# Performance work log

Measured on AMD Instinct MI355X. Metric: run time of the kernel, lower is better.

The kernel has to match this reference:

```python
import jax, jax.numpy as jnp
import numpy as np

B, C, A = 4, 8, 9            # batch, num_classes, anchors per location
IMG = 512.0                   # image spatial size (square)
FEATS = [64, 32, 16, 8, 4]    # FPN feature map sizes
STRIDES = [8, 16, 32, 64, 128]
TOPK = 1000                   # topk_candidates_per_level
SCORE_THRESH = 0.05
NMS_THRESH = 0.5
DETS = 300                    # detections_per_img
BBOX_CLIP = float(np.log(1000.0 / 16.0))  # standard BoxCoder dw/dh clamp


def _make_anchors(f, stride):
    # 3 aspect ratios x 3 octave scales = 9 anchors per location (torchvision-style)
    base = stride * 4.0
    ratios = np.array([0.5, 1.0, 2.0])
    scales = np.array([2.0 ** 0, 2.0 ** (1.0 / 3.0), 2.0 ** (2.0 / 3.0)])
    ws, hs = [], []
    for r in ratios:
        for sc in scales:
            area = (base * sc) ** 2
            w = np.sqrt(area / r)
            ws.append(w)
            hs.append(w * r)
    ws = np.array(ws)
    hs = np.array(hs)
    shifts = (np.arange(f) + 0.5) * stride
    cx, cy = np.meshgrid(shifts, shifts, indexing='ij')  # H-major, matches map flatten
    cx = cx.reshape(-1)[:, None]
    cy = cy.reshape(-1)[:, None]
    boxes = np.stack([cx - ws / 2, cy - hs / 2, cx + ws / 2, cy + hs / 2], axis=-1)
    return boxes.reshape(-1, 4).astype(np.float32)  # [f*f*A, 4], location-major


def setup_inputs() -> dict:
    key = jax.random.key(0)
    inp = {}
    for i, (f, s) in enumerate(zip(FEATS, STRIDES)):
        k1 = jax.random.fold_in(key, 2 * i)
        k2 = jax.random.fold_in(key, 2 * i + 1)
        inp[f'cls_{i}'] = jax.random.normal(k1, (B, C * A, f, f), jnp.float32)
        inp[f'reg_{i}'] = 0.2 * jax.random.normal(k2, (B, 4 * A, f, f), jnp.float32)
        inp[f'anchors_{i}'] = jnp.asarray(_make_anchors(f, s))
    return inp


def _decode(reg, anc):
    # BoxCoder.decode with weights (1,1,1,1)
    aw = anc[..., 2] - anc[..., 0]
    ah = anc[..., 3] - anc[..., 1]
    acx = anc[..., 0] + 0.5 * aw
    acy = anc[..., 1] + 0.5 * ah
    dx, dy = reg[..., 0], reg[..., 1]
    dw = jnp.minimum(reg[..., 2], BBOX_CLIP)
    dh = jnp.minimum(reg[..., 3], BBOX_CLIP)
    pcx = dx * aw + acx
    pcy = dy * ah + acy
    pw = jnp.exp(dw) * aw
    ph = jnp.exp(dh) * ah
    boxes = jnp.stack([pcx - 0.5 * pw, pcy - 0.5 * ph, pcx + 0.5 * pw, pcy + 0.5 * ph], axis=-1)
    return jnp.clip(boxes, 0.0, IMG)  # clip_boxes_to_image


def _level_select(cls_map, reg_map, anchors):
    b, _, h, w = cls_map.shape
    # (B, A*C, H, W) -> (B, H*W*A, C) -> flat (B, H*W*A*C)
    logits = cls_map.reshape(b, A, C, h, w).transpose(0, 3, 4, 1, 2).reshape(b, -1)
    scores = jax.nn.sigmoid(logits)
    regs = reg_map.reshape(b, A, 4, h, w).transpose(0, 3, 4, 1, 2).reshape(b, -1, 4)
    top_s, top_i = jax.lax.top_k(scores, TOPK)  # topk_candidates_per_level
    anc_idx = top_i // C
    labels = top_i % C
    sel_reg = jnp.take_along_axis(regs, anc_idx[..., None], axis=1)  # [B,K,4]
    sel_anc = anchors[anc_idx]                                        # [B,K,4]
    boxes = _decode(sel_reg, sel_anc)
    top_s = jnp.where(top_s > SCORE_THRESH, top_s, -1.0)  # score threshold -> invalid
    return boxes, top_s, labels


def _pairwise_iou(a, b):
    lt = jnp.maximum(a[:, None, :2], b[None, :, :2])
    rb = jnp.minimum(a[:, None, 2:], b[None, :, 2:])
    wh = jnp.clip(rb - lt, 0.0)
    inter = wh[..., 0] * wh[..., 1]
    area_a = (a[:, 2] - a[:, 0]) * (a[:, 3] - a[:, 1])
    area_b = (b[:, 2] - b[:, 0]) * (b[:, 3] - b[:, 1])
    return inter / jnp.maximum(area_a[:, None] + area_b[None, :] - inter, 1e-7)


def _nms_image(boxes, scores, labels):
    # class-aware NMS via per-class coordinate offset (batched_nms trick)
    order = jnp.argsort(-scores)
    b = boxes[order]
    s = scores[order]
    l = labels[order]
    ob = b + (l.astype(b.dtype) * (IMG + 1.0))[:, None]
    iou = _pairwise_iou(jax.lax.stop_gradient(ob), jax.lax.stop_gradient(ob))
    n = s.shape[0]
    idxs = jnp.arange(n)
    def body(i, keep):
        sup = (iou[i] > NMS_THRESH) & keep[i] & (idxs > i)
        return keep & (~sup)
    keep = jax.lax.fori_loop(0, n, body, s > 0.0)
    s2 = jnp.where(keep, s, -1.0)
    top_s, idx = jax.lax.top_k(s2, DETS)  # detections_per_img
    valid = top_s > 0.0
    out_boxes = jnp.where(valid[:, None], b[idx], 0.0)
    out_scores = jnp.maximum(top_s, 0.0)
    out_labels = jnp.where(valid, l[idx], -1)
    return out_boxes, out_scores, out_labels


def reference(cls_0, cls_1, cls_2, cls_3, cls_4,
              reg_0, reg_1, reg_2, reg_3, reg_4,
              anchors_0, anchors_1, anchors_2, anchors_3, anchors_4):
    levels = [
        (cls_0, reg_0, anchors_0), (cls_1, reg_1, anchors_1),
        (cls_2, reg_2, anchors_2), (cls_3, reg_3, anchors_3),
        (cls_4, reg_4, anchors_4),
    ]
    outs = [_level_select(c, r, a) for c, r, a in levels]
    boxes = jnp.concatenate([o[0] for o in outs], axis=1)   # [B, 5*TOPK, 4]
    scores = jnp.concatenate([o[1] for o in outs], axis=1)  # [B, 5*TOPK]
    labels = jnp.concatenate([o[2] for o in outs], axis=1)
    return jax.vmap(_nms_image)(boxes, scores, labels)  # boxes [B,300,4], scores [B,300], labels [B,300]
```

## Files before the change

### kernel.cpp

```cpp
#include <hip/hip_runtime.h>
#include <stdint.h>
#include <stddef.h>

typedef unsigned int u32;
typedef unsigned long long u64;
typedef unsigned short u16;
typedef unsigned char u8;

#define NB 4
#define NLEV 5
#define NCH 72
#define NREGCH 36
#define TOPK 1000
#define NCAND 5000
#define NDET 300
#define NBINS 16384
#define RNB 4096
#define CAP 8192
#define FASTCAP 2048
#define CHUNK 8192
#define NCHUNK_IMG 50
#define DCH 512
#define DW 8
#define IMGSZ 512.0f
#define SCORE_TH 0.05f
#define NMS_TH 0.5f
#define BBOX_CLIP_F 4.135166556742356f

__constant__ int c_f[NLEV]    = {64, 32, 16, 8, 4};
__constant__ int c_Nloc[NLEV] = {4096, 1024, 256, 64, 16};
__constant__ int c_lg2[NLEV]  = {12, 10, 8, 6, 4};
__constant__ float c_tau[NLEV] = {2.594f, 2.075f, 1.433f, 0.513f, -1e30f};
__constant__ int c_rshift[NLEV] = {10, 10, 11, 12, 18};

__device__ __forceinline__ float xla_tanh_f32(float x) {
  float ax = fabsf(x);
  float xc = fminf(fmaxf(x, -7.90531110763549805f), 7.90531110763549805f);
  float x2 = __fmul_rn(xc, xc);
  float p = -2.76076847742355e-16f;
  p = __fadd_rn(__fmul_rn(x2, p), 2.00018790482477e-13f);
  p = __fadd_rn(__fmul_rn(x2, p), -8.60467152213735e-11f);
  p = __fadd_rn(__fmul_rn(x2, p), 5.12229709037114e-08f);
  p = __fadd_rn(__fmul_rn(x2, p), 1.48572235717979e-05f);
  p = __fadd_rn(__fmul_rn(x2, p), 6.37261928875436e-04f);
  p = __fadd_rn(__fmul_rn(x2, p), 4.89352455891786e-03f);
  float num = __fmul_rn(xc, p);
  float q = 1.19825839466702e-06f;
  q = __fadd_rn(__fmul_rn(x2, q), 1.18534705686654e-04f);
  q = __fadd_rn(__fmul_rn(x2, q), 2.26843463243900e-03f);
  q = __fadd_rn(__fmul_rn(x2, q), 4.89352518554385e-03f);
  float r = __fdiv_rn(num, q);
  return (ax < 0.0004f) ? x : r;
}
__device__ __forceinline__ float sigmoid_ref(float x) {
  return __fadd_rn(0.5f, __fmul_rn(0.5f, xla_tanh_f32(__fmul_rn(0.5f, x))));
}

struct ClsPtrs { const float* p[NLEV]; };
struct LevelPtrs { const float* reg[NLEV]; const float* anc[NLEV]; };

__device__ __forceinline__ void chunk_map(int bid, int& b, int& level, int& chunk) {
  b = bid / NCHUNK_IMG;
  int cid = bid % NCHUNK_IMG;
  if      (cid < 36) { level = 0; chunk = cid; }
  else if (cid < 45) { level = 1; chunk = cid - 36; }
  else if (cid < 48) { level = 2; chunk = cid - 45; }
  else if (cid < 49) { level = 3; chunk = cid - 48; }
  else               { level = 4; chunk = cid - 49; }
}

__device__ __forceinline__ float4 decode_box(const LevelPtrs& lp, int b, int lv, u32 e) {
  u32 anc = e >> 3;
  int a = (int)(anc % 9u);
  int loc = (int)(anc / 9u);
  int f = c_f[lv];
  int Nloc = f * f;
  const float* rp = lp.reg[lv];
  const float* ap = lp.anc[lv] + (size_t)anc * 4;
  float r0 = rp[((size_t)b * NREGCH + (a * 4 + 0)) * Nloc + loc];
  float r1 = rp[((size_t)b * NREGCH + (a * 4 + 1)) * Nloc + loc];
  float r2 = rp[((size_t)b * NREGCH + (a * 4 + 2)) * Nloc + loc];
  float r3 = rp[((size_t)b * NREGCH + (a * 4 + 3)) * Nloc + loc];
  float a0 = ap[0], a1 = ap[1], a2 = ap[2], a3 = ap[3];
  float aw = __fsub_rn(a2, a0);
  float ah = __fsub_rn(a3, a1);
  float acx = __fadd_rn(a0, __fmul_rn(0.5f, aw));
  float acy = __fadd_rn(a1, __fmul_rn(0.5f, ah));
  float dw = fminf(r2, BBOX_CLIP_F);
  float dh = fminf(r3, BBOX_CLIP_F);
  float pcx = __fadd_rn(__fmul_rn(r0, aw), acx);
  float pcy = __fadd_rn(__fmul_rn(r1, ah), acy);
  float pw = __fmul_rn(expf(dw), aw);
  float ph = __fmul_rn(expf(dh), ah);
  float hx = __fmul_rn(0.5f, pw);
  float hy = __fmul_rn(0.5f, ph);
  float4 v;
  v.x = fminf(fmaxf(__fsub_rn(pcx, hx), 0.0f), IMGSZ);
  v.y = fminf(fmaxf(__fsub_rn(pcy, hy), 0.0f), IMGSZ);
  v.z = fminf(fmaxf(__fadd_rn(pcx, hx), 0.0f), IMGSZ);
  v.w = fminf(fmaxf(__fadd_rn(pcy, hy), 0.0f), IMGSZ);
  return v;
}

__global__ __launch_bounds__(256)
void k_filter(ClsPtrs cp, u32* __restrict__ selcnt, u64* __restrict__ sel) {
  int b, level, chunk;
  chunk_map(blockIdx.x, b, level, chunk);
  int Nloc = c_Nloc[level], lg2 = c_lg2[level];
  int Nsc = Nloc * NCH;
  int g = b * NLEV + level;
  const float* cls = cp.p[level] + (size_t)b * Nsc;
  float tau = c_tau[level];
  int base = chunk * CHUNK;
  int end = base + CHUNK; if (end > Nsc) end = Nsc;
  int wid = threadIdx.x >> 6, lane = threadIdx.x & 63;
  u64 lowm = (1ull << lane) - 1ull;
  __shared__ u32 wcnt[4];
  __shared__ u32 s_gbase;
  u32 mycnt = 0;
  for (int i = base + threadIdx.x; i < end; i += 256) {
    u64 mk = __ballot((int)(cls[i] > tau));
    mycnt += (u32)__popcll(mk);
  }
  if (lane == 0) wcnt[wid] = mycnt;
  __syncthreads();
  u32 wbase = 0, tot = 0;
  for (int w = 0; w < 4; ++w) { u32 c = wcnt[w]; if (w < wid) wbase += c; tot += c; }
  if (threadIdx.x == 0 && tot) s_gbase = atomicAdd(&selcnt[g], tot);
  __syncthreads();
  if (!tot) return;
  u32 gb = s_gbase;
  u32 run = 0;
  for (int i = base + threadIdx.x; i < end; i += 256) {
    float x = cls[i];
    bool selp = x > tau;
    u64 mk = __ballot((int)selp);
    if (selp) {
      u32 pos = gb + wbase + run + (u32)__popcll(mk & lowm);
      if (pos < CAP) {
        u32 bits = __float_as_uint(sigmoid_ref(x));
        int ch = i >> lg2;
        int loc = i & (Nloc - 1);
        u32 e = (u32)(loc * NCH + ch);
        sel[(size_t)g * CAP + pos] = ((u64)bits << 32) | (u32)(~e);
      }
    }
    run += (u32)__popcll(mk);
  }
}

__global__ __launch_bounds__(1024)
void k_rank(ClsPtrs cp, LevelPtrs lp, const u32* __restrict__ selcnt,
            const u64* __restrict__ sel,
            float* __restrict__ cand_s, u32* __restrict__ cand_t,
            float4* __restrict__ cand_box) {
  __shared__ union {
    struct { u64 keys2[FASTCAP]; u32 hist[RNB]; u32 pfx[RNB]; } f;
    u32 histfb[NBINS];
    u64 keysfb[CAP];
  } sh;
  __shared__ u32 part[1024];
  __shared__ u32 s_last;
  __shared__ u32 s_cnt;
  __shared__ int s_cut;
  int g = blockIdx.x;
  int b = g / NLEV, l = g % NLEV;
  int Nloc = c_Nloc[l], lg2 = c_lg2[l];
  int Nsc = Nloc * NCH;
  int tid = threadIdx.x;
  int lane = tid & 63;
  u64 lowm = (1ull << lane) - 1ull;
  int obase = b * NCAND + l * TOPK;
  u32 cnt = selcnt[g];
  bool fast = (cnt >= TOPK) && (cnt <= FASTCAP);
  if (fast) {
    u32 m = cnt;
    int shift = c_rshift[l];
    for (int i = tid; i < RNB; i += 1024) { sh.f.hist[i] = 0; }
    if (tid == 0) s_last = 0;
    u64 k0a = ((u32)tid < m)        ? sel[(size_t)g * CAP + tid]        : 0ULL;
    u64 k0b = ((u32)tid + 1024 < m) ? sel[(size_t)g * CAP + tid + 1024] : 0ULL;
    auto bkt_of = [&](u64 k) -> int {
      int d = (int)0x3F800000 - (int)(u32)(k >> 32);
      if (d < 0) d = 0;
      int bq = d >> shift;
      return bq > RNB - 1 ? RNB - 1 : bq;
    };
    int ba = bkt_of(k0a), bb = bkt_of(k0b);
    __syncthreads();
    if ((u32)tid < m)        atomicAdd(&sh.f.hist[ba], 1u);
    if ((u32)tid + 1024 < m) atomicAdd(&sh.f.hist[bb], 1u);
    __syncthreads();
    {
      int t4 = tid * 4;
      u32 h0 = sh.f.hist[t4], h1 = sh.f.hist[t4 + 1], h2 = sh.f.hist[t4 + 2], h3 = sh.f.hist[t4 + 3];
      u32 s4 = h0 + h1 + h2 + h3;
      u32 x = s4;
      for (int d = 1; d < 64; d <<= 1) { u32 y = __shfl_up(x, d); if (lane >= d) x += y; }
      if (lane == 63) part[tid >> 6] = x;
      __syncthreads();
      if (tid == 0) { u32 a = 0; for (int w = 0; w < 16; ++w) { u32 c = part[w]; part[w] = a; a += c; } }
      __syncthreads();
      u32 base2 = part[tid >> 6] + (x - s4);
      sh.f.pfx[t4]     = base2;
      sh.f.pfx[t4 + 1] = base2 + h0;
      sh.f.pfx[t4 + 2] = base2 + h0 + h1;
      sh.f.pfx[t4 + 3] = base2 + h0 + h1 + h2;
    }
    __syncthreads();
    if ((u32)tid < m)        { u32 p = atomicAdd(&sh.f.pfx[ba], 1u); sh.f.keys2[p] = k0a; }
    if ((u32)tid + 1024 < m) { u32 p = atomicAdd(&sh.f.pfx[bb], 1u); sh.f.keys2[p] = k0b; }
    __syncthreads();
    auto emit = [&](u64 k0, int bkt) {
      u32 endq = sh.f.pfx[bkt];
      u32 startq = endq - sh.f.hist[bkt];
      u32 r = startq;
      for (u32 j = startq; j < endq; ++j) r += (sh.f.keys2[j] > k0) ? 1u : 0u;
      if (r < TOPK) {
        u32 hi = (u32)(k0 >> 32);
        cand_s[obase + r] = __uint_as_float(hi);
        u32 e = ~((u32)k0);
        cand_t[obase + r] = ((u32)l << 19) | (e & 0x7FFFFu);
        cand_box[obase + r] = decode_box(lp, b, l, e);
        if (r == TOPK - 1) s_last = hi;
      }
    };
    if ((u32)tid < m)        emit(k0a, ba);
    if ((u32)tid + 1024 < m) emit(k0b, bb);
    __syncthreads();
    u32 bits_tau = __float_as_uint(sigmoid_ref(c_tau[l]));
    if ((int)cnt != Nsc && !(s_last > bits_tau + 64u)) fast = false;
  }
  if (fast) return;

  const float* cls = cp.p[l] + (size_t)b * Nsc;
  __syncthreads();
  for (int i = tid; i < NBINS; i += 1024) sh.histfb[i] = 0;
  if (tid == 0) s_cnt = 0;
  __syncthreads();
  for (int i = tid; i < Nsc; i += 1024) {
    float s = sigmoid_ref(cls[i]);
    atomicAdd(&sh.histfb[__float_as_uint(s) >> 16], 1u);
  }
  __syncthreads();
  { u32 a = 0; for (int j = 0; j < 16; ++j) a += sh.histfb[tid * 16 + j]; part[tid] = a; }
  __syncthreads();
  if (tid == 0) {
    u32 cum = 0; int cut = 0;
    for (int ch = 1023; ch >= 0; --ch) {
      if (cum + part[ch] >= TOPK) {
        u32 cc = cum;
        for (int bin = ch * 16 + 15;; --bin) { cc += sh.histfb[bin]; if (cc >= TOPK) { cut = bin; break; } }
        break;
      }
      cum += part[ch];
    }
    s_cut = cut;
  }
  __syncthreads();
  int cut = s_cut;
  __syncthreads();
  for (int i = tid; i < Nsc; i += 1024) {
    float s = sigmoid_ref(cls[i]);
    u32 bits = __float_as_uint(s);
    bool selp = (int)(bits >> 16) >= cut;
    u64 mk = __ballot((int)selp);
    if (selp) {
      int ldr = __builtin_ctzll(mk);
      u32 pos0 = 0;
      if (lane == ldr) pos0 = atomicAdd(&s_cnt, (u32)__popcll(mk));
      pos0 = (u32)__shfl((int)pos0, ldr);
      u32 pos = pos0 + (u32)__popcll(mk & lowm);
      if (pos < CAP) {
        int ch = i >> lg2;
        int loc = i & (Nloc - 1);
        u32 e = (u32)(loc * NCH + ch);
        sh.keysfb[pos] = ((u64)bits << 32) | (u32)(~e);
      }
    }
  }
  __syncthreads();
  u32 m2 = s_cnt; if (m2 > CAP) m2 = CAP;
  for (u32 i = tid; i < m2; i += 1024) {
    u64 k0 = sh.keysfb[i];
    u32 r = 0;
    #pragma unroll 8
    for (u32 j = 0; j < m2; ++j) r += (sh.keysfb[j] > k0) ? 1u : 0u;
    if (r < TOPK) {
      cand_s[obase + r] = __uint_as_float((u32)(k0 >> 32));
      u32 e = ~((u32)k0);
      cand_t[obase + r] = ((u32)l << 19) | (e & 0x7FFFFu);
      cand_box[obase + r] = decode_box(lp, b, l, e);
    }
  }
  for (u32 r = m2 + tid; r < TOPK; r += 1024) {
    cand_s[obase + r] = -1.0f;
    cand_t[obase + r] = ((u32)l << 19) | r;
    cand_box[obase + r] = make_float4(0.f, 0.f, 0.f, 0.f);
  }
}

__global__ __launch_bounds__(1024)
void k_grank(const float* __restrict__ cand_s, const u32* __restrict__ cand_t,
             const float4* __restrict__ cand_box, u32* __restrict__ invCnt,
             float4* __restrict__ rboxOff, u32* __restrict__ rmeta) {
  __shared__ u64 keys[NCAND];
  int b = blockIdx.y;
  int seg = blockIdx.x;
  int tid = threadIdx.x;
  for (int i = tid; i < NCAND; i += 1024) {
    float s = cand_s[b * NCAND + i];
    u32 t = cand_t[b * NCAND + i];
    u32 hi = (s > SCORE_TH) ? __float_as_uint(s) : 0u;
    keys[i] = ((u64)hi << 32) | (u32)(~t);
  }
  __syncthreads();
  if (tid >= TOPK) return;
  int i = seg * TOPK + tid;
  u64 k0 = keys[i];
  u32 hi = (u32)(k0 >> 32);
  u32 t = ~((u32)k0);
  int rank;
  u32 cls = 0;
  if (hi) {
    rank = tid;
    for (int L = 0; L < NLEV; ++L) {
      if (L == seg) continue;
      const u64* A = keys + L * TOPK;
      int lo = 0, h2 = TOPK;
      while (lo < h2) { int mid = (lo + h2) >> 1; if (A[mid] > k0) lo = mid + 1; else h2 = mid; }
      rank += lo;
    }
    cls = t & 7u;
  } else {
    rank = (NCAND - 1) - (int)atomicAdd(&invCnt[b], 1u);
  }
  float4 v = cand_box[b * NCAND + i];
  float off = __fmul_rn((float)cls, IMGSZ + 1.0f);
  float4 q;
  q.x = __fadd_rn(v.x, off); q.y = __fadd_rn(v.y, off);
  q.z = __fadd_rn(v.z, off); q.w = __fadd_rn(v.w, off);
  rboxOff[b * NCAND + rank] = q;
  rmeta[b * NCAND + rank] = hi ? (((u32)i << 8) | cls) : 0xFFFFFFFFu;
}

__device__ __forceinline__ bool iou_gt4(float4 p, float pa, float4 q, float qa) {
  float ltx = fmaxf(p.x, q.x), lty = fmaxf(p.y, q.y);
  float rx  = fminf(p.z, q.z), ry  = fminf(p.w, q.w);
  float ww = fmaxf(__fsub_rn(rx, ltx), 0.0f);
  float hh = fmaxf(__fsub_rn(ry, lty), 0.0f);
  float inter = __fmul_rn(ww, hh);
  bool res = false;
  if (inter > 0.0f) {
    float denom = fmaxf(__fsub_rn(__fadd_rn(pa, qa), inter), 1e-7f);
    res = __fdiv_rn(inter, denom) > NMS_TH;
  }
  return res;
}
__device__ __forceinline__ float area_rn(float4 p) {
  return __fmul_rn(__fsub_rn(p.z, p.x), __fsub_rn(p.w, p.y));
}

__global__ __launch_bounds__(256)
void k_mask(const float4* __restrict__ rboxOff, u64* __restrict__ rowsG) {
  __shared__ float4 sb[DCH];
  __shared__ float  sa[DCH];
  int b = blockIdx.y, rb = blockIdx.x;
  int tid = threadIdx.x;
  for (int i = tid; i < DCH; i += 256) {
    float4 q = rboxOff[b * NCAND + i];
    sb[i] = q; sa[i] = area_rn(q);
  }
  __syncthreads();
  int lane = tid & 63, wv = tid >> 6;
  int r = rb * 64 + lane;
  float4 qr = sb[r]; float ar = sa[r];
  u64* rowp = rowsG + ((size_t)b * DCH + r) * DW;
  for (int w = wv; w < rb; w += 4) rowp[w] = 0;
  for (int w = rb + wv; w < DW; w += 4) {
    u64 bits = 0;
    int j0 = w * 64;
    if (w > rb) {
      #pragma unroll 4
      for (int jc = 0; jc < 64; ++jc)
        if (iou_gt4(qr, ar, sb[j0 + jc], sa[j0 + jc])) bits |= 1ull << jc;
    } else {
      #pragma unroll 4
      for (int jc = 0; jc < 64; ++jc) {
        int j = j0 + jc;
        if (j > r && iou_gt4(qr, ar, sb[j], sa[j])) bits |= 1ull << jc;
      }
    }
    rowp[w] = bits;
  }
}

__global__ __launch_bounds__(1024)
void k_detect(const float* __restrict__ cand_s, const float4* __restrict__ cand_box,
              const float4* __restrict__ rboxOff, const u32* __restrict__ rmeta,
              const u64* __restrict__ rowsG, float* __restrict__ out) {
  __shared__ u64 rows[DCH][DW];
  __shared__ u32 sm[DCH];
  __shared__ u32 nzmap[DCH / 32];
  __shared__ u64 validm[DW], keptm[DW];
  __shared__ float4 kbox[NDET];
  __shared__ float  karea2[NDET];
  __shared__ u32    kmeta[NDET];
  __shared__ float4 cbox[64];
  __shared__ float  carea[64];
  __shared__ u64    supsh[16];
  __shared__ u32 s_nk, s_stop;
  int b = blockIdx.x, tid = threadIdx.x;
  int lane = tid & 63, wid = tid >> 6;
  if (tid < DCH / 32) nzmap[tid] = 0;
  if (tid == 0) { s_nk = 0; s_stop = 0; }
  __syncthreads();
  for (int k = tid; k < DCH * DW; k += 1024) {
    u64 v = rowsG[(size_t)b * DCH * DW + k];
    ((u64*)rows)[k] = v;
    if (v) atomicOr(&nzmap[(k / DW) >> 5], 1u << ((k / DW) & 31));
  }
  if (tid < DCH) sm[tid] = rmeta[b * NCAND + tid];
  __syncthreads();
  if (tid < DCH) {
    u64 bv = __ballot((int)(sm[tid] != 0xFFFFFFFFu));
    if (lane == 0) validm[tid >> 6] = bv;
  }
  __syncthreads();
  if (tid == 0) {
    u64 kw[DW];
    #pragma unroll
    for (int w = 0; w < DW; ++w) kw[w] = validm[w];
    for (int mw = 0; mw < DCH / 32; ++mw) {
      u32 nzw = nzmap[mw];
      while (nzw) {
        int bit = __builtin_ctz(nzw); nzw &= nzw - 1;
        int i = mw * 32 + bit;
        if ((kw[i >> 6] >> (i & 63)) & 1ull) {
          #pragma unroll
          for (int v = 0; v < DW; ++v) kw[v] &= ~rows[i][v];
        }
      }
    }
    #pragma unroll
    for (int w = 0; w < DW; ++w) keptm[w] = kw[w];
  }
  __syncthreads();
  if (tid < DCH) {
    int w = tid >> 6;
    u64 kwv = keptm[w];
    if ((kwv >> (tid & 63)) & 1ull) {
      u32 pre = 0;
      for (int v = 0; v < w; ++v) pre += (u32)__popcll(keptm[v]);
      pre += (u32)__popcll(kwv & ((1ull << (tid & 63)) - 1ull));
      if (pre < NDET) {
        float4 q = rboxOff[b * NCAND + tid];
        kbox[pre] = q; karea2[pre] = area_rn(q); kmeta[pre] = sm[tid];
      }
    }
  }
  __syncthreads();
  if (tid == 0) {
    u32 add = 0, nvalid = 0;
    #pragma unroll
    for (int w = 0; w < DW; ++w) { add += (u32)__popcll(keptm[w]); nvalid += (u32)__popcll(validm[w]); }
    u32 nn = add; if (nn > NDET) nn = NDET;
    s_nk = nn;
    if (nn >= (u32)NDET || nvalid < (u32)DCH) s_stop = 1;
  }
  __syncthreads();

  int n = (int)s_nk;
  for (int base = DCH; base < NCAND && !s_stop; base += 64) {
    int ci = base + lane;
    u32 meta = (ci < NCAND) ? rmeta[b * NCAND + ci] : 0xFFFFFFFFu;
    bool valid = meta != 0xFFFFFFFFu;
    float4 q = (ci < NCAND) ? rboxOff[b * NCAND + ci] : make_float4(0.f, 0.f, 0.f, 0.f);
    float aq = area_rn(q);
    if (wid == 0) { cbox[lane] = q; carea[lane] = aq; }
    bool sup = false;
    if (valid) for (int k = wid; k < n; k += 16) sup = sup | iou_gt4(kbox[k], karea2[k], q, aq);
    u64 bal = __ballot((int)sup);
    if (lane == 0) supsh[wid] = bal;
    __syncthreads();
    if (wid == 0) {
      u64 supm = 0;
      for (int w = 0; w < 16; ++w) supm |= supsh[w];
      u64 vm = __ballot((int)valid);
      u64 pending = vm & ~supm;
      u64 row = 0;
      if ((pending >> lane) & 1ull) {
        u64 mine = pending & ~((2ull << lane) - 1ull);
        while (mine) {
          int j = __builtin_ctzll(mine); mine &= mine - 1ull;
          if (iou_gt4(q, aq, cbox[j], carea[j])) row |= (1ull << j);
        }
      }
      __shared__ u64 rowsh2[64];
      rowsh2[lane] = row;
      u64 nz = __ballot((int)(row != 0ull));
      bool done = false;
      u64 rem = pending;
      while (rem) {
        int r = __builtin_ctzll(rem); rem &= rem - 1ull;
        if (lane == r) { kmeta[n] = meta; kbox[n] = q; karea2[n] = aq; }
        ++n;
        if (n == NDET) { done = true; break; }
        if ((nz >> r) & 1ull) rem &= ~rowsh2[r];
      }
      if (__any((int)(!valid))) done = true;
      if (lane == 0) { s_nk = (u32)n; s_stop = done ? 1u : 0u; }
    }
    __syncthreads();
    n = (int)s_nk;
  }

  int nf = (int)s_nk;
  for (int k = tid; k < NDET; k += 1024) {
    float bx0 = 0.f, bx1 = 0.f, bx2 = 0.f, bx3 = 0.f, sc = 0.f, lb = -1.0f;
    if (k < nf) {
      u32 m = kmeta[k];
      int io = (int)(m >> 8);
      float4 v = cand_box[b * NCAND + io];
      bx0 = v.x; bx1 = v.y; bx2 = v.z; bx3 = v.w;
      sc = cand_s[b * NCAND + io];
      lb = (float)(m & 0xFFu);
    }
    int idx = b * NDET + k;
    out[(size_t)idx * 4 + 0] = bx0;
    out[(size_t)idx * 4 + 1] = bx1;
    out[(size_t)idx * 4 + 2] = bx2;
    out[(size_t)idx * 4 + 3] = bx3;
    out[NB * NDET * 4 + idx] = sc;
    out[NB * NDET * 5 + idx] = lb;
  }
}

extern "C" void kernel_launch(void* const* d_in, const int* in_sizes, int n_in,
                              void* d_out, int out_size, void* d_ws, size_t ws_size,
                              hipStream_t stream) {
  const float* cls[NLEV]; const float* reg[NLEV]; const float* anc[NLEV];
  bool dict_order = (n_in >= 2) && (in_sizes[1] == 4 * NREGCH * 64 * 64);
  for (int l = 0; l < NLEV; ++l) {
    if (dict_order) {
      cls[l] = (const float*)d_in[3 * l + 0];
      reg[l] = (const float*)d_in[3 * l + 1];
      anc[l] = (const float*)d_in[3 * l + 2];
    } else {
      cls[l] = (const float*)d_in[l];
      reg[l] = (const float*)d_in[NLEV + l];
      anc[l] = (const float*)d_in[2 * NLEV + l];
    }
  }

  char* ws = (char*)d_ws;
  size_t off = 0;
  auto alloc = [&](size_t bytes) -> void* {
    void* p = ws + off;
    off = (off + bytes + 255) & ~(size_t)255;
    return p;
  };
  u32*    ctrs     = (u32*)   alloc(24 * 4);
  u64*    sel      = (u64*)   alloc(20ULL * CAP * 8);
  float*  cand_s   = (float*) alloc((size_t)NB * NCAND * 4);
  u32*    cand_t   = (u32*)   alloc((size_t)NB * NCAND * 4);
  float4* cand_box = (float4*)alloc((size_t)NB * NCAND * 16);
  float4* rboxOff  = (float4*)alloc((size_t)NB * NCAND * 16);
  u32*    rmeta    = (u32*)   alloc((size_t)NB * NCAND * 4);
  u64*    rowsG    = (u64*)   alloc((size_t)NB * DCH * DW * 8);
  (void)ws_size; (void)out_size;

  u32* selcnt = ctrs;
  u32* invCnt = ctrs + 20;
  hipMemsetAsync(ctrs, 0, 24 * 4, stream);

  ClsPtrs cp;
  for (int l = 0; l < NLEV; ++l) cp.p[l] = cls[l];
  LevelPtrs lp;
  for (int l = 0; l < NLEV; ++l) { lp.reg[l] = reg[l]; lp.anc[l] = anc[l]; }

  k_filter<<<NB * NCHUNK_IMG, 256, 0, stream>>>(cp, selcnt, sel);
  k_rank<<<NB * NLEV, 1024, 0, stream>>>(cp, lp, selcnt, sel, cand_s, cand_t, cand_box);
  k_grank<<<dim3(NLEV, NB), 1024, 0, stream>>>(cand_s, cand_t, cand_box, invCnt, rboxOff, rmeta);
  k_mask<<<dim3(DW, NB), 256, 0, stream>>>(rboxOff, rowsG);
  k_detect<<<NB, 1024, 0, stream>>>(cand_s, cand_box, rboxOff, rmeta, rowsG, (float*)d_out);
}
```

Measured before the change: 63.79 us.

## Replace global atomic counters with per-chunk regions and deterministic ranks

The filter kernel now writes per-block counts and stores selected candidates into a fixed per-chunk region, so it no longer needs a global atomicAdd or a second block barrier. The rank kernel gathers the chunk regions into shared memory using a prefix over the chunk counts, and it handles per-chunk overflow by falling back to the slow path. Invalid candidates in the grank kernel get ranks from per-level valid counts found by binary search, which removes the atomic counter and lets the memset launch be dropped. The cost is an extra gather pass into shared memory and larger shared memory use in k_rank.

```diff
diff --git a/kernel.cpp b/kernel.cpp
--- a/kernel.cpp
+++ b/kernel.cpp
@@ -32,6 +32,9 @@
 __constant__ int c_lg2[NLEV]  = {12, 10, 8, 6, 4};
 __constant__ float c_tau[NLEV] = {2.594f, 2.075f, 1.433f, 0.513f, -1e30f};
 __constant__ int c_rshift[NLEV] = {10, 10, 11, 12, 18};
+__constant__ int c_nch[NLEV]  = {36, 9, 3, 1, 1};
+__constant__ int c_clo[NLEV]  = {0, 36, 45, 48, 49};
+__constant__ int c_ccap[NLEV] = {227, 910, 2730, 8192, 8192};
 
 __device__ __forceinline__ float xla_tanh_f32(float x) {
   float ax = fabsf(x);
@@ -103,7 +106,7 @@
 }
 
 __global__ __launch_bounds__(256)
-void k_filter(ClsPtrs cp, u32* __restrict__ selcnt, u64* __restrict__ sel) {
+void k_filter(ClsPtrs cp, u32* __restrict__ bcnt, u64* __restrict__ sel) {
   int b, level, chunk;
   chunk_map(blockIdx.x, b, level, chunk);
   int Nloc = c_Nloc[level], lg2 = c_lg2[level];
@@ -116,7 +119,6 @@
   int wid = threadIdx.x >> 6, lane = threadIdx.x & 63;
   u64 lowm = (1ull << lane) - 1ull;
   __shared__ u32 wcnt[4];
-  __shared__ u32 s_gbase;
   u32 mycnt = 0;
   for (int i = base + threadIdx.x; i < end; i += 256) {
     u64 mk = __ballot((int)(cls[i] > tau));
@@ -126,23 +128,23 @@
   __syncthreads();
   u32 wbase = 0, tot = 0;
   for (int w = 0; w < 4; ++w) { u32 c = wcnt[w]; if (w < wid) wbase += c; tot += c; }
-  if (threadIdx.x == 0 && tot) s_gbase = atomicAdd(&selcnt[g], tot);
-  __syncthreads();
+  if (threadIdx.x == 0) bcnt[blockIdx.x] = tot;
   if (!tot) return;
-  u32 gb = s_gbase;
+  u32 ccap = (u32)c_ccap[level];
+  size_t regbase = (size_t)g * CAP + (size_t)chunk * ccap;
   u32 run = 0;
   for (int i = base + threadIdx.x; i < end; i += 256) {
     float x = cls[i];
     bool selp = x > tau;
     u64 mk = __ballot((int)selp);
     if (selp) {
-      u32 pos = gb + wbase + run + (u32)__popcll(mk & lowm);
-      if (pos < CAP) {
+      u32 pos = wbase + run + (u32)__popcll(mk & lowm);
+      if (pos < ccap) {
         u32 bits = __float_as_uint(sigmoid_ref(x));
         int ch = i >> lg2;
         int loc = i & (Nloc - 1);
         u32 e = (u32)(loc * NCH + ch);
-        sel[(size_t)g * CAP + pos] = ((u64)bits << 32) | (u32)(~e);
+        sel[regbase + pos] = ((u64)bits << 32) | (u32)(~e);
       }
     }
     run += (u32)__popcll(mk);
@@ -150,16 +152,19 @@
 }
 
 __global__ __launch_bounds__(1024)
-void k_rank(ClsPtrs cp, LevelPtrs lp, const u32* __restrict__ selcnt,
+void k_rank(ClsPtrs cp, LevelPtrs lp, const u32* __restrict__ bcnt,
             const u64* __restrict__ sel,
             float* __restrict__ cand_s, u32* __restrict__ cand_t,
             float4* __restrict__ cand_box) {
   __shared__ union {
-    struct { u64 keys2[FASTCAP]; u32 hist[RNB]; u32 pfx[RNB]; } f;
+    struct { u64 keysC[FASTCAP]; u64 keys2[FASTCAP]; u32 hist[RNB]; u32 pfx[RNB]; } f;
     u32 histfb[NBINS];
     u64 keysfb[CAP];
   } sh;
   __shared__ u32 part[1024];
+  __shared__ u32 ccnt[36];
+  __shared__ u32 cbase[37];
+  __shared__ u32 s_ovf;
   __shared__ u32 s_last;
   __shared__ u32 s_cnt;
   __shared__ int s_cut;
@@ -171,15 +176,31 @@
   int lane = tid & 63;
   u64 lowm = (1ull << lane) - 1ull;
   int obase = b * NCAND + l * TOPK;
-  u32 cnt = selcnt[g];
-  bool fast = (cnt >= TOPK) && (cnt <= FASTCAP);
+  int nch = c_nch[l], clo = c_clo[l];
+  u32 ccap = (u32)c_ccap[l];
+  if (tid < nch) ccnt[tid] = bcnt[b * NCHUNK_IMG + clo + tid];
+  __syncthreads();
+  if (tid == 0) {
+    u32 a = 0, ovf = 0;
+    for (int c = 0; c < nch; ++c) { cbase[c] = a; a += ccnt[c]; if (ccnt[c] > ccap) ovf = 1; }
+    cbase[nch] = a; s_ovf = ovf;
+  }
+  __syncthreads();
+  u32 cnt = cbase[nch];
+  bool fast = (cnt >= TOPK) && (cnt <= FASTCAP) && !s_ovf;
   if (fast) {
     u32 m = cnt;
     int shift = c_rshift[l];
-    for (int i = tid; i < RNB; i += 1024) { sh.f.hist[i] = 0; }
+    for (int c = 0; c < nch; ++c) {
+      u32 cc = ccnt[c], cb2 = cbase[c];
+      for (u32 i = tid; i < cc; i += 1024)
+        sh.f.keysC[cb2 + i] = sel[(size_t)g * CAP + (size_t)c * ccap + i];
+    }
+    for (int i = tid; i < RNB; i += 1024) sh.f.hist[i] = 0;
     if (tid == 0) s_last = 0;
-    u64 k0a = ((u32)tid < m)        ? sel[(size_t)g * CAP + tid]        : 0ULL;
-    u64 k0b = ((u32)tid + 1024 < m) ? sel[(size_t)g * CAP + tid + 1024] : 0ULL;
+    __syncthreads();
+    u64 k0a = ((u32)tid < m)        ? sh.f.keysC[tid]        : 0ULL;
+    u64 k0b = ((u32)tid + 1024 < m) ? sh.f.keysC[tid + 1024] : 0ULL;
     auto bkt_of = [&](u64 k) -> int {
       int d = (int)0x3F800000 - (int)(u32)(k >> 32);
       if (d < 0) d = 0;
@@ -187,7 +208,6 @@
       return bq > RNB - 1 ? RNB - 1 : bq;
     };
     int ba = bkt_of(k0a), bb = bkt_of(k0b);
-    __syncthreads();
     if ((u32)tid < m)        atomicAdd(&sh.f.hist[ba], 1u);
     if ((u32)tid + 1024 < m) atomicAdd(&sh.f.hist[bb], 1u);
     __syncthreads();
@@ -302,9 +322,10 @@
 
 __global__ __launch_bounds__(1024)
 void k_grank(const float* __restrict__ cand_s, const u32* __restrict__ cand_t,
-             const float4* __restrict__ cand_box, u32* __restrict__ invCnt,
+             const float4* __restrict__ cand_box,
              float4* __restrict__ rboxOff, u32* __restrict__ rmeta) {
   __shared__ u64 keys[NCAND];
+  __shared__ int vc[NLEV];
   int b = blockIdx.y;
   int seg = blockIdx.x;
   int tid = threadIdx.x;
@@ -313,6 +334,13 @@
     u32 t = cand_t[b * NCAND + i];
     u32 hi = (s > SCORE_TH) ? __float_as_uint(s) : 0u;
     keys[i] = ((u64)hi << 32) | (u32)(~t);
+  }
+  __syncthreads();
+  if (tid < NLEV) {
+    const u64* A = keys + tid * TOPK;
+    int lo = 0, h2 = TOPK;
+    while (lo < h2) { int mid = (lo + h2) >> 1; if (A[mid] >> 32) lo = mid + 1; else h2 = mid; }
+    vc[tid] = lo;
   }
   __syncthreads();
   if (tid >= TOPK) return;
@@ -333,7 +361,9 @@
     }
     cls = t & 7u;
   } else {
-    rank = (NCAND - 1) - (int)atomicAdd(&invCnt[b], 1u);
+    int tv = 0, before = 0;
+    for (int L = 0; L < NLEV; ++L) { tv += vc[L]; if (L < seg) before += TOPK - vc[L]; }
+    rank = tv + before + (tid - vc[seg]);
   }
   float4 v = cand_box[b * NCAND + i];
   float off = __fmul_rn((float)cls, IMGSZ + 1.0f);
@@ -560,7 +590,7 @@
     off = (off + bytes + 255) & ~(size_t)255;
     return p;
   };
-  u32*    ctrs     = (u32*)   alloc(24 * 4);
+  u32*    bcnt     = (u32*)   alloc((size_t)NB * NCHUNK_IMG * 4);
   u64*    sel      = (u64*)   alloc(20ULL * CAP * 8);
   float*  cand_s   = (float*) alloc((size_t)NB * NCAND * 4);
   u32*    cand_t   = (u32*)   alloc((size_t)NB * NCAND * 4);
@@ -570,18 +600,14 @@
   u64*    rowsG    = (u64*)   alloc((size_t)NB * DCH * DW * 8);
   (void)ws_size; (void)out_size;
 
-  u32* selcnt = ctrs;
-  u32* invCnt = ctrs + 20;
-  hipMemsetAsync(ctrs, 0, 24 * 4, stream);
-
   ClsPtrs cp;
   for (int l = 0; l < NLEV; ++l) cp.p[l] = cls[l];
   LevelPtrs lp;
   for (int l = 0; l < NLEV; ++l) { lp.reg[l] = reg[l]; lp.anc[l] = anc[l]; }
 
-  k_filter<<<NB * NCHUNK_IMG, 256, 0, stream>>>(cp, selcnt, sel);
-  k_rank<<<NB * NLEV, 1024, 0, stream>>>(cp, lp, selcnt, sel, cand_s, cand_t, cand_box);
-  k_grank<<<dim3(NLEV, NB), 1024, 0, stream>>>(cand_s, cand_t, cand_box, invCnt, rboxOff, rmeta);
+  k_filter<<<NB * NCHUNK_IMG, 256, 0, stream>>>(cp, bcnt, sel);
+  k_rank<<<NB * NLEV, 1024, 0, stream>>>(cp, lp, bcnt, sel, cand_s, cand_t, cand_box);
+  k_grank<<<dim3(NLEV, NB), 1024, 0, stream>>>(cand_s, cand_t, cand_box, rboxOff, rmeta);
   k_mask<<<dim3(DW, NB), 256, 0, stream>>>(rboxOff, rowsG);
   k_detect<<<NB, 1024, 0, stream>>>(cand_s, cand_box, rboxOff, rmeta, rowsG, (float*)d_out);
 }
```

Result: slower. 69.96 us (+9.7%).
